# Kernel optimization log

Hardware: AMD Instinct MI355X
Metric: run time of the kernel (lower is better)

## Reference

```python
import jax, jax.numpy as jnp
import numpy as np

DECAY = 0.7      # membrane decay
THETA = 1.0      # spike threshold
K_WINNERS = 5
GAIN_UP = 1.5
GAIN_DOWN = 0.6

SEQ_LEN = 8192
VOCAB = 128000


def setup_inputs() -> dict:
    key = jax.random.key(0)
    token_seq = jax.random.randint(key, (SEQ_LEN,), 0, VOCAB)  # int token ids
    v0 = jnp.zeros((VOCAB,), jnp.float32)  # initial membrane potentials
    return {"token_seq": token_seq, "v0": v0, "vocab_size": VOCAB}


def reference(token_seq, v0, vocab_size):
    spikes0 = jnp.zeros((vocab_size,), jnp.float32)

    def lif_step(state, token_id):
        v, spikes = state
        t = jnp.clip(token_id, 0, vocab_size - 1).astype(jnp.int32)
        v_new = DECAY * v[t] + 1.0                      # gather + decay + input current
        spiked = v_new >= THETA
        v = v.at[t].set(jnp.where(spiked, v_new - THETA, v_new))  # reset-by-subtraction
        spikes = spikes.at[t].add(spiked.astype(jnp.float32))
        return (v, spikes), None

    (v_final, spikes_final), _ = jax.lax.scan(lif_step, (v0, spikes0), token_seq)

    k = min(K_WINNERS, int(vocab_size))
    _, top_idx = jax.lax.top_k(v_final, k)
    winners = jnp.zeros((vocab_size,), jnp.float32).at[top_idx].set(1.0)
    gains = jnp.where(winners > 0, GAIN_UP,
                      jnp.where(spikes_final > 0, GAIN_DOWN, 1.0))
    return gains
```

## Files before the change

### kernel.cpp

```cpp
#include <hip/hip_runtime.h>
#include <float.h>
#include <limits.h>

#define DECAY 0.7f
#define THETA 1.0f
#define KWIN 5
#define GAIN_UP 1.5f
#define GAIN_DOWN 0.6f

#define NT 256
#define SLICE 1024
#define WPB (NT / 64)
#define CPB (WPB * KWIN)
#define MAXC 10

__device__ __forceinline__ void lif_replay(float v0, int n, float& v_out, int& spikes_out) {
    float v = v0;
    int s = 0;
    for (int i = 0; i < n; ++i) {
        float vn = __fadd_rn(__fmul_rn(DECAY, v), 1.0f);
        if (vn >= THETA) { v = __fsub_rn(vn, THETA); ++s; }
        else             { v = vn; }
    }
    v_out = v;
    spikes_out = s;
}

__device__ __forceinline__ void better(float& bv, int& bi, float ov, int oi) {
    if (ov > bv || (ov == bv && oi < bi)) { bv = ov; bi = oi; }
}

__device__ __forceinline__ unsigned long long mkkey(float v, int idx) {
    unsigned b  = __float_as_uint(v);
    unsigned sv = (b & 0x80000000u) ? ~b : (b | 0x80000000u);
    return ((unsigned long long)sv << 32) | (unsigned)(~(unsigned)idx);
}

__global__ __launch_bounds__(NT) void fused_spin(const int* __restrict__ tok,
                                                 const float* __restrict__ v0,
                                                 int n, int vocab,
                                                 float* __restrict__ out,
                                                 unsigned long long* __restrict__ A,
                                                 unsigned long long* __restrict__ B,
                                                 int nb) {
    __shared__ int hist[SLICE];
    __shared__ unsigned long long cl[CPB];
    __shared__ unsigned long long swk[WPB];

    const int tid  = threadIdx.x;
    const int bid  = blockIdx.x;
    const int wave = tid >> 6;
    const int lane = tid & 63;
    const int sbase = bid * SLICE;

    #pragma unroll
    for (int k = 0; k < SLICE / NT; ++k) {
        hist[k * NT + tid] = 0;
    }
    __syncthreads();

    int nv4 = n & ~3;
    for (int j = tid * 4; j < nv4; j += NT * 4) {
        int4 t4 = *(const int4*)(tok + j);
        int t; unsigned r;
        t = min(max(t4.x, 0), vocab - 1); r = (unsigned)(t - sbase); if (r < SLICE) atomicAdd(&hist[r], 1);
        t = min(max(t4.y, 0), vocab - 1); r = (unsigned)(t - sbase); if (r < SLICE) atomicAdd(&hist[r], 1);
        t = min(max(t4.z, 0), vocab - 1); r = (unsigned)(t - sbase); if (r < SLICE) atomicAdd(&hist[r], 1);
        t = min(max(t4.w, 0), vocab - 1); r = (unsigned)(t - sbase); if (r < SLICE) atomicAdd(&hist[r], 1);
    }
    for (int j = nv4 + tid; j < n; j += NT) {
        int t = min(max(tok[j], 0), vocab - 1);
        unsigned r = (unsigned)(t - sbase);
        if (r < SLICE) atomicAdd(&hist[r], 1);
    }
    __syncthreads();

    const int wbase = wave * 256;
    float lv[4];
    int   li[4];
    #pragma unroll
    for (int k = 0; k < 4; ++k) {
        int off = wbase + k * 64 + lane;
        int idx = sbase + off;
        float vf = -FLT_MAX;
        int   id = -1;
        if (idx < vocab) {
            int c = hist[off];
            int s;
            lif_replay(v0[idx], c, vf, s);
            out[idx] = (s > 0) ? GAIN_DOWN : 1.0f;
            id = idx;
        }
        lv[k] = vf;
        li[k] = id;
    }

    #pragma unroll
    for (int r = 0; r < KWIN; ++r) {
        float bv = -FLT_MAX;
        int   bi = INT_MAX;
        #pragma unroll
        for (int k = 0; k < 4; ++k) {
            if (li[k] >= 0) better(bv, bi, lv[k], li[k]);
        }
        #pragma unroll
        for (int off = 32; off > 0; off >>= 1) {
            float ov = __shfl_xor(bv, off, 64);
            int   oi = __shfl_xor(bi, off, 64);
            better(bv, bi, ov, oi);
        }
        if (lane == 0) {
            cl[wave * KWIN + r] = (bi == INT_MAX) ? 0ULL : mkkey(bv, bi);
        }
        #pragma unroll
        for (int k = 0; k < 4; ++k) {
            if (li[k] == bi) li[k] = -1;
        }
    }
    __syncthreads();

    if (wave == 0) {
        __threadfence();
        if (lane < CPB) {
            int j = bid * CPB + lane;
            unsigned long long key = cl[lane];
            __hip_atomic_store(&A[j], key,  __ATOMIC_RELAXED, __HIP_MEMORY_SCOPE_AGENT);
            __hip_atomic_store(&B[j], ~key, __ATOMIC_RELAXED, __HIP_MEMORY_SCOPE_AGENT);
        }
    }

    if (bid != 0) return;

    const int n_cand = nb * CPB;
    unsigned long long k0 = 0ULL, k1 = 0ULL, k2 = 0ULL, k3 = 0ULL, k4 = 0ULL;
    unsigned long long k5 = 0ULL, k6 = 0ULL, k7 = 0ULL, k8 = 0ULL, k9 = 0ULL;
    #pragma unroll
    for (int s = 0; s < MAXC; ++s) {
        int j = s * NT + tid;
        unsigned long long key = 0ULL;
        if (j < n_cand) {
            for (;;) {
                unsigned long long a = __hip_atomic_load(&A[j], __ATOMIC_RELAXED, __HIP_MEMORY_SCOPE_AGENT);
                unsigned long long b = __hip_atomic_load(&B[j], __ATOMIC_RELAXED, __HIP_MEMORY_SCOPE_AGENT);
                if (b == ~a) { key = a; break; }
                __builtin_amdgcn_s_sleep(2);
            }
        }
        if (s == 0) k0 = key; else if (s == 1) k1 = key;
        else if (s == 2) k2 = key; else if (s == 3) k3 = key;
        else if (s == 4) k4 = key; else if (s == 5) k5 = key;
        else if (s == 6) k6 = key; else if (s == 7) k7 = key;
        else if (s == 8) k8 = key; else k9 = key;
    }
    __threadfence();

    unsigned long long thresh = ~0ULL;
    for (int r = 0; r < KWIN; ++r) {
        unsigned long long best = 0ULL;
        if (k0 < thresh && k0 > best) best = k0;
        if (k1 < thresh && k1 > best) best = k1;
        if (k2 < thresh && k2 > best) best = k2;
        if (k3 < thresh && k3 > best) best = k3;
        if (k4 < thresh && k4 > best) best = k4;
        if (k5 < thresh && k5 > best) best = k5;
        if (k6 < thresh && k6 > best) best = k6;
        if (k7 < thresh && k7 > best) best = k7;
        if (k8 < thresh && k8 > best) best = k8;
        if (k9 < thresh && k9 > best) best = k9;

        #pragma unroll
        for (int off = 32; off > 0; off >>= 1) {
            unsigned hi  = (unsigned)(best >> 32);
            unsigned lo  = (unsigned)(best & 0xFFFFFFFFu);
            unsigned ohi = __shfl_xor(hi, off, 64);
            unsigned olo = __shfl_xor(lo, off, 64);
            unsigned long long ok = ((unsigned long long)ohi << 32) | olo;
            if (ok > best) best = ok;
        }
        if (lane == 0) swk[wave] = best;
        __syncthreads();

        unsigned long long bb = swk[0];
        if (swk[1] > bb) bb = swk[1];
        if (swk[2] > bb) bb = swk[2];
        if (swk[3] > bb) bb = swk[3];
        __syncthreads();

        if (tid == 0 && bb != 0ULL) {
            int idx = (int)(~(unsigned)(bb & 0xFFFFFFFFu));
            out[idx] = GAIN_UP;
        }
        thresh = bb;
    }
}

extern "C" void kernel_launch(void* const* d_in, const int* in_sizes, int n_in,
                              void* d_out, int out_size, void* d_ws, size_t ws_size,
                              hipStream_t stream) {
    const int*   tok = (const int*)d_in[0];
    const float* v0  = (const float*)d_in[1];
    int n     = in_sizes[0];
    int vocab = in_sizes[1];
    float* out = (float*)d_out;

    int nb = (vocab + SLICE - 1) / SLICE;
    unsigned long long* A = (unsigned long long*)d_ws;
    unsigned long long* B = A + (size_t)nb * CPB;

    fused_spin<<<nb, NT, 0, stream>>>(tok, v0, n, vocab, out, A, B, nb);
}
```

Baseline: 72.78 us.

## Make every block redundantly compute the global top-k and write only its own winners

Every block now publishes its five-per-wave candidates and then waits on the full candidate set. Each block computes the global top-k itself, instead of funnelling the final reduction through block 0. A block writes GAIN_UP only for winners inside its own vocab slice, so writes to `out` no longer cross blocks and the thread fences can go. The spin-wait now issues all candidate loads up front before polling, which overlaps their latency. The cost is redundant reduction work and extra L2 traffic from every block polling the whole candidate array, and all blocks must still be co-resident.

```diff
diff --git a/kernel.cpp b/kernel.cpp
--- a/kernel.cpp
+++ b/kernel.cpp
@@ -36,13 +36,13 @@
     return ((unsigned long long)sv << 32) | (unsigned)(~(unsigned)idx);
 }
 
-__global__ __launch_bounds__(NT) void fused_spin(const int* __restrict__ tok,
-                                                 const float* __restrict__ v0,
-                                                 int n, int vocab,
-                                                 float* __restrict__ out,
-                                                 unsigned long long* __restrict__ A,
-                                                 unsigned long long* __restrict__ B,
-                                                 int nb) {
+__global__ __launch_bounds__(NT) void fused_sym(const int* __restrict__ tok,
+                                                const float* __restrict__ v0,
+                                                int n, int vocab,
+                                                float* __restrict__ out,
+                                                unsigned long long* __restrict__ A,
+                                                unsigned long long* __restrict__ B,
+                                                int nb) {
     __shared__ int hist[SLICE];
     __shared__ unsigned long long cl[CPB];
     __shared__ unsigned long long swk[WPB];
@@ -119,54 +119,47 @@
     }
     __syncthreads();
 
-    if (wave == 0) {
-        __threadfence();
-        if (lane < CPB) {
-            int j = bid * CPB + lane;
-            unsigned long long key = cl[lane];
-            __hip_atomic_store(&A[j], key,  __ATOMIC_RELAXED, __HIP_MEMORY_SCOPE_AGENT);
-            __hip_atomic_store(&B[j], ~key, __ATOMIC_RELAXED, __HIP_MEMORY_SCOPE_AGENT);
-        }
-    }
-
-    if (bid != 0) return;
+    if (lane < KWIN) {
+        int c = wave * KWIN + lane;
+        int j = bid * CPB + c;
+        unsigned long long key = cl[c];
+        __hip_atomic_store(&A[j], key,  __ATOMIC_RELAXED, __HIP_MEMORY_SCOPE_AGENT);
+        __hip_atomic_store(&B[j], ~key, __ATOMIC_RELAXED, __HIP_MEMORY_SCOPE_AGENT);
+    }
 
     const int n_cand = nb * CPB;
-    unsigned long long k0 = 0ULL, k1 = 0ULL, k2 = 0ULL, k3 = 0ULL, k4 = 0ULL;
-    unsigned long long k5 = 0ULL, k6 = 0ULL, k7 = 0ULL, k8 = 0ULL, k9 = 0ULL;
+    unsigned long long av[MAXC], bw[MAXC], key_[MAXC];
     #pragma unroll
     for (int s = 0; s < MAXC; ++s) {
         int j = s * NT + tid;
-        unsigned long long key = 0ULL;
+        av[s] = 0ULL; bw[s] = ~0ULL;
         if (j < n_cand) {
-            for (;;) {
-                unsigned long long a = __hip_atomic_load(&A[j], __ATOMIC_RELAXED, __HIP_MEMORY_SCOPE_AGENT);
-                unsigned long long b = __hip_atomic_load(&B[j], __ATOMIC_RELAXED, __HIP_MEMORY_SCOPE_AGENT);
-                if (b == ~a) { key = a; break; }
-                __builtin_amdgcn_s_sleep(2);
+            av[s] = __hip_atomic_load(&A[j], __ATOMIC_RELAXED, __HIP_MEMORY_SCOPE_AGENT);
+            bw[s] = __hip_atomic_load(&B[j], __ATOMIC_RELAXED, __HIP_MEMORY_SCOPE_AGENT);
+        }
+    }
+    #pragma unroll
+    for (int s = 0; s < MAXC; ++s) {
+        int j = s * NT + tid;
+        if (j < n_cand) {
+            while (bw[s] != ~av[s]) {
+                __builtin_amdgcn_s_sleep(1);
+                av[s] = __hip_atomic_load(&A[j], __ATOMIC_RELAXED, __HIP_MEMORY_SCOPE_AGENT);
+                bw[s] = __hip_atomic_load(&B[j], __ATOMIC_RELAXED, __HIP_MEMORY_SCOPE_AGENT);
             }
-        }
-        if (s == 0) k0 = key; else if (s == 1) k1 = key;
-        else if (s == 2) k2 = key; else if (s == 3) k3 = key;
-        else if (s == 4) k4 = key; else if (s == 5) k5 = key;
-        else if (s == 6) k6 = key; else if (s == 7) k7 = key;
-        else if (s == 8) k8 = key; else k9 = key;
-    }
-    __threadfence();
+            key_[s] = av[s];
+        } else {
+            key_[s] = 0ULL;
+        }
+    }
 
     unsigned long long thresh = ~0ULL;
     for (int r = 0; r < KWIN; ++r) {
         unsigned long long best = 0ULL;
-        if (k0 < thresh && k0 > best) best = k0;
-        if (k1 < thresh && k1 > best) best = k1;
-        if (k2 < thresh && k2 > best) best = k2;
-        if (k3 < thresh && k3 > best) best = k3;
-        if (k4 < thresh && k4 > best) best = k4;
-        if (k5 < thresh && k5 > best) best = k5;
-        if (k6 < thresh && k6 > best) best = k6;
-        if (k7 < thresh && k7 > best) best = k7;
-        if (k8 < thresh && k8 > best) best = k8;
-        if (k9 < thresh && k9 > best) best = k9;
+        #pragma unroll
+        for (int s = 0; s < MAXC; ++s) {
+            if (key_[s] < thresh && key_[s] > best) best = key_[s];
+        }
 
         #pragma unroll
         for (int off = 32; off > 0; off >>= 1) {
@@ -188,7 +181,7 @@
 
         if (tid == 0 && bb != 0ULL) {
             int idx = (int)(~(unsigned)(bb & 0xFFFFFFFFu));
-            out[idx] = GAIN_UP;
+            if ((unsigned)(idx - sbase) < SLICE) out[idx] = GAIN_UP;
         }
         thresh = bb;
     }
@@ -207,5 +200,5 @@
     unsigned long long* A = (unsigned long long*)d_ws;
     unsigned long long* B = A + (size_t)nb * CPB;
 
-    fused_spin<<<nb, NT, 0, stream>>>(tok, v0, n, vocab, out, A, B, nb);
-}
+    fused_sym<<<nb, NT, 0, stream>>>(tok, v0, n, vocab, out, A, B, nb);
+}
```

Result: no change. 72.41 us (-0.5%).
